# Performance work log

Measured on AMD Instinct MI355X. Metric: run time of the kernel, lower is better.

Reference implementation:

```python
import jax, jax.numpy as jnp
import numpy as np

D = 1024
H = 16
DK = D // H
MLP = 4096
EPS = 1e-5


def layernorm(x, w, b):
    mu = jnp.mean(x, axis=-1, keepdims=True)
    var = jnp.mean(jnp.square(x - mu), axis=-1, keepdims=True)
    return (x - mu) * jax.lax.rsqrt(var + EPS) * w + b


def setup_inputs() -> dict:
    key = jax.random.key(0)
    ks = jax.random.split(key, 12)
    s = 0.02
    return {
        "x": jax.random.normal(ks[0], (8, 1024, D), dtype=jnp.float32),
        "ln1_w": jnp.ones((D,), jnp.float32),
        "ln1_b": jnp.zeros((D,), jnp.float32),
        "wq": jax.random.normal(ks[1], (D, D), jnp.float32) * s,
        "bq": jnp.zeros((D,), jnp.float32),
        "wk": jax.random.normal(ks[2], (D, D), jnp.float32) * s,
        "bk": jnp.zeros((D,), jnp.float32),
        "wv": jax.random.normal(ks[3], (D, D), jnp.float32) * s,
        "bv": jnp.zeros((D,), jnp.float32),
        "wo": jax.random.normal(ks[4], (D, D), jnp.float32) * s,
        "bo": jnp.zeros((D,), jnp.float32),
        "ln2_w": jnp.ones((D,), jnp.float32),
        "ln2_b": jnp.zeros((D,), jnp.float32),
        "w1": jax.random.normal(ks[5], (D, MLP), jnp.float32) * s,
        "b1": jnp.zeros((MLP,), jnp.float32),
        "w2": jax.random.normal(ks[6], (MLP, D), jnp.float32) * s,
        "b2": jnp.zeros((D,), jnp.float32),
    }


def reference(x, ln1_w, ln1_b, wq, bq, wk, bk, wv, bv, wo, bo, ln2_w, ln2_b, w1, b1, w2, b2):
    B, S, _ = x.shape
    h = layernorm(x, ln1_w, ln1_b)
    # QKV projections, split heads: [B, H, S, DK]
    q = (h @ wq + bq).reshape(B, S, H, DK).transpose(0, 2, 1, 3)
    k = (h @ wk + bk).reshape(B, S, H, DK).transpose(0, 2, 1, 3)
    v = (h @ wv + bv).reshape(B, S, H, DK).transpose(0, 2, 1, 3)
    scores = jnp.einsum('bhqd,bhkd->bhqk', q, k) / np.sqrt(DK).astype(np.float32)
    attn = jax.nn.softmax(scores, axis=-1)
    ctx = jnp.einsum('bhqk,bhkd->bhqd', attn, v)
    ctx = ctx.transpose(0, 2, 1, 3).reshape(B, S, D)
    # NOTE: original MultiHeadAttention applies ReLU after the output projection
    attn_out = jax.nn.relu(ctx @ wo + bo)
    out1 = x + attn_out  # dropout is identity in eval
    h2 = layernorm(out1, ln2_w, ln2_b)
    ff = jax.nn.gelu(h2 @ w1 + b1, approximate=False) @ w2 + b2
    return out1 + ff
```

## Files before the change

kernel.cpp:

```cpp
#include <hip/hip_runtime.h>
#include <hip/hip_bf16.h>
#include <math.h>

typedef __bf16 bf16x8 __attribute__((ext_vector_type(8)));
typedef float f32x4 __attribute__((ext_vector_type(4)));

typedef __attribute__((address_space(3))) unsigned int lds_u32_t;
typedef __attribute__((address_space(1))) const unsigned int glb_u32_t;

static __device__ __forceinline__ f32x4 mfma16(bf16x8 a, bf16x8 b, f32x4 c) {
  return __builtin_amdgcn_mfma_f32_16x16x32_bf16(a, b, c, 0, 0, 0);
}

static __device__ __forceinline__ void load_lds16(const __bf16* g, __bf16* l) {
  __builtin_amdgcn_global_load_lds((glb_u32_t*)g, (lds_u32_t*)l, 16, 0, 0);
}

__global__ __launch_bounds__(256) void transpose_w(const float* __restrict__ src,
                                                   __bf16* __restrict__ dst,
                                                   int R, int C) {
  __shared__ float tile[32][33];
  int tx = threadIdx.x, ty = threadIdx.y;
  int c0 = blockIdx.x * 32, r0 = blockIdx.y * 32;
#pragma unroll
  for (int i = 0; i < 4; i++)
    tile[ty + 8 * i][tx] = src[(size_t)(r0 + ty + 8 * i) * C + c0 + tx];
  __syncthreads();
#pragma unroll
  for (int i = 0; i < 4; i++)
    dst[(size_t)(c0 + ty + 8 * i) * R + r0 + tx] = (__bf16)tile[tx][ty + 8 * i];
}

__global__ __launch_bounds__(256) void ln_kernel(const float* __restrict__ x,
                                                 const float* __restrict__ w,
                                                 const float* __restrict__ b,
                                                 __bf16* __restrict__ out) {
  int row = blockIdx.x, tid = threadIdx.x;
  const float* xr = x + (size_t)row * 1024;
  float v[4];
  float s = 0.f, sq = 0.f;
#pragma unroll
  for (int i = 0; i < 4; i++) {
    v[i] = xr[tid + 256 * i];
    s += v[i];
    sq += v[i] * v[i];
  }
#pragma unroll
  for (int off = 1; off < 64; off <<= 1) {
    s += __shfl_xor(s, off, 64);
    sq += __shfl_xor(sq, off, 64);
  }
  __shared__ float red[8];
  int wave = tid >> 6, lane = tid & 63;
  if (lane == 0) { red[wave] = s; red[4 + wave] = sq; }
  __syncthreads();
  if (tid == 0) {
    float S = red[0] + red[1] + red[2] + red[3];
    float SQ = red[4] + red[5] + red[6] + red[7];
    float mu = S * (1.f / 1024.f);
    float var = SQ * (1.f / 1024.f) - mu * mu;
    red[0] = mu;
    red[1] = rsqrtf(var + 1e-5f);
  }
  __syncthreads();
  float mu = red[0], rstd = red[1];
  __bf16* orow = out + (size_t)row * 1024;
#pragma unroll
  for (int i = 0; i < 4; i++) {
    int c = tid + 256 * i;
    orow[c] = (__bf16)((v[i] - mu) * rstd * w[c] + b[c]);
  }
}

enum { MODE_QKV = 0, MODE_WO = 3, MODE_F1 = 4, MODE_F2 = 5 };

template <int MODE>
__global__ __launch_bounds__(256, 2) void gemm_bt(const __bf16* __restrict__ A,
                                                  const __bf16* __restrict__ Bt,
                                                  const float* __restrict__ b0,
                                                  const float* __restrict__ b1,
                                                  const float* __restrict__ b2,
                                                  const float* __restrict__ aux,
                                                  void* __restrict__ o0,
                                                  void* __restrict__ o1,
                                                  void* __restrict__ o2,
                                                  int N, int K) {
  __shared__ __align__(16) __bf16 As[128 * 64];
  __shared__ __align__(16) __bf16 Bs[128 * 64];
  const int tid = threadIdx.x;
  const int m0 = blockIdx.y * 128, n0 = blockIdx.x * 128;
  const int wave = tid >> 6, lane = tid & 63, quad = lane >> 4, l16 = lane & 15;
  const int wm = (wave >> 1) * 64, wn = (wave & 1) * 64;

  int srow[4], sgran[4];
#pragma unroll
  for (int i = 0; i < 4; i++) {
    int inst = wave * 4 + i;
    srow[i] = inst * 8 + (lane >> 3);
    sgran[i] = (lane & 7) ^ (srow[i] & 7);
  }

  const f32x4 zero4 = {0.f, 0.f, 0.f, 0.f};
  f32x4 acc[4][4];
#pragma unroll
  for (int i = 0; i < 4; i++)
#pragma unroll
    for (int j = 0; j < 4; j++) acc[i][j] = zero4;

  for (int kt = 0; kt < K; kt += 64) {
#pragma unroll
    for (int i = 0; i < 4; i++) {
      int inst = wave * 4 + i;
      load_lds16(&A[(size_t)(m0 + srow[i]) * K + kt + sgran[i] * 8], &As[inst * 512]);
      load_lds16(&Bt[(size_t)(n0 + srow[i]) * K + kt + sgran[i] * 8], &Bs[inst * 512]);
    }
    __syncthreads();
#pragma unroll
    for (int ks = 0; ks < 64; ks += 32) {
      bf16x8 af[4], bfv[4];
#pragma unroll
      for (int mi = 0; mi < 4; mi++) {
        int row = wm + 16 * mi + l16;
        int pg = ((ks >> 3) + quad) ^ (row & 7);
        af[mi] = *(const bf16x8*)&As[row * 64 + pg * 8];
      }
#pragma unroll
      for (int ni = 0; ni < 4; ni++) {
        int row = wn + 16 * ni + l16;
        int pg = ((ks >> 3) + quad) ^ (row & 7);
        bfv[ni] = *(const bf16x8*)&Bs[row * 64 + pg * 8];
      }
#pragma unroll
      for (int mi = 0; mi < 4; mi++)
#pragma unroll
        for (int ni = 0; ni < 4; ni++)
          acc[mi][ni] = mfma16(af[mi], bfv[ni], acc[mi][ni]);
    }
    __syncthreads();
  }

  int seg = (n0 >> 10);
  const float* bsel = (MODE == MODE_QKV) ? (seg == 0 ? b0 : seg == 1 ? b1 : b2) : b0;

#pragma unroll
  for (int mi = 0; mi < 4; mi++) {
#pragma unroll
    for (int ni = 0; ni < 4; ni++) {
      int ncol = n0 + wn + 16 * ni + l16;
      int cc = ncol & 1023;
      float bval = bsel[(MODE == MODE_QKV) ? cc : ncol];
#pragma unroll
      for (int r = 0; r < 4; r++) {
        int m = m0 + wm + 16 * mi + quad * 4 + r;
        float val = acc[mi][ni][r] + bval;
        if constexpr (MODE == MODE_QKV) {
          int bb = m >> 10, s = m & 1023, h = cc >> 6, dk = cc & 63;
          if (seg == 0)
            ((__bf16*)o0)[(((size_t)(bb * 16 + h)) * 1024 + s) * 64 + dk] =
                (__bf16)(val * 0.125f);
          else if (seg == 1)
            ((__bf16*)o1)[(((size_t)(bb * 16 + h)) * 1024 + s) * 64 + dk] = (__bf16)val;
          else
            ((__bf16*)o2)[(((size_t)(bb * 16 + h)) * 64 + dk) * 1024 + s] = (__bf16)val;
        } else if constexpr (MODE == MODE_WO) {
          val = fmaxf(val, 0.f);
          size_t idx = (size_t)m * 1024 + ncol;
          ((float*)o0)[idx] = aux[idx] + val;
        } else if constexpr (MODE == MODE_F1) {
          float g = 0.5f * val * (1.f + erff(val * 0.70710678118654752f));
          ((__bf16*)o0)[(size_t)m * 4096 + ncol] = (__bf16)g;
        } else {
          size_t idx = (size_t)m * 1024 + ncol;
          ((float*)o0)[idx] = aux[idx] + val;
        }
      }
    }
  }
}

__global__ __launch_bounds__(256) void attn_kernel(const __bf16* __restrict__ Q,
                                                   const __bf16* __restrict__ Kp,
                                                   const __bf16* __restrict__ Vt,
                                                   __bf16* __restrict__ ctx) {
  __shared__ __align__(16) __bf16 Ps[128][72];
  const int tid = threadIdx.x;
  const int bh = blockIdx.x, qb = blockIdx.y;
  const int wave = tid >> 6, lane = tid & 63, quad = lane >> 4, l16 = lane & 15;
  const int qrow0 = qb * 128 + wave * 32;

  bf16x8 aq[2][2];
#pragma unroll
  for (int mi = 0; mi < 2; mi++) {
    const __bf16* qrow = Q + ((size_t)bh * 1024 + qrow0 + mi * 16 + l16) * 64;
    aq[mi][0] = *(const bf16x8*)&qrow[8 * quad];
    aq[mi][1] = *(const bf16x8*)&qrow[32 + 8 * quad];
  }

  const f32x4 zero4 = {0.f, 0.f, 0.f, 0.f};
  f32x4 o[2][4];
  float lp[2][4];
#pragma unroll
  for (int mi = 0; mi < 2; mi++)
#pragma unroll
    for (int i = 0; i < 4; i++) { o[mi][i] = zero4; lp[mi][i] = 0.f; }

  const __bf16* kb0 = Kp + (size_t)bh * 65536;
  const __bf16* vb0 = Vt + (size_t)bh * 65536;

  bf16x8 kfA[4][2], kfB[4][2];
#pragma unroll
  for (int ni = 0; ni < 4; ni++) {
    const __bf16* krow = kb0 + (16 * ni + l16) * 64;
    kfA[ni][0] = *(const bf16x8*)&krow[8 * quad];
    kfA[ni][1] = *(const bf16x8*)&krow[32 + 8 * quad];
  }

  auto body = [&](int kbk, bf16x8 (&kcur)[4][2], bf16x8 (&knxt)[4][2]) {
    bf16x8 vf[4][2];
#pragma unroll
    for (int ni = 0; ni < 4; ni++) {
      const __bf16* vrow = vb0 + (size_t)(16 * ni + l16) * 1024 + kbk * 64;
      vf[ni][0] = *(const bf16x8*)&vrow[8 * quad];
      vf[ni][1] = *(const bf16x8*)&vrow[32 + 8 * quad];
    }
    if (kbk < 15) {
      const __bf16* kbase = kb0 + (kbk + 1) * 4096;
#pragma unroll
      for (int ni = 0; ni < 4; ni++) {
        const __bf16* krow = kbase + (16 * ni + l16) * 64;
        knxt[ni][0] = *(const bf16x8*)&krow[8 * quad];
        knxt[ni][1] = *(const bf16x8*)&krow[32 + 8 * quad];
      }
    }
    f32x4 s[2][4];
#pragma unroll
    for (int mi = 0; mi < 2; mi++)
#pragma unroll
      for (int ni = 0; ni < 4; ni++) {
        s[mi][ni] = mfma16(aq[mi][0], kcur[ni][0], zero4);
        s[mi][ni] = mfma16(aq[mi][1], kcur[ni][1], s[mi][ni]);
      }
#pragma unroll
    for (int mi = 0; mi < 2; mi++)
#pragma unroll
      for (int ni = 0; ni < 4; ni++)
#pragma unroll
        for (int r = 0; r < 4; r++) {
          float p = __expf(s[mi][ni][r]);
          lp[mi][r] += p;
          Ps[wave * 32 + mi * 16 + quad * 4 + r][16 * ni + l16] = (__bf16)p;
        }
    bf16x8 pa[2][2];
#pragma unroll
    for (int mi = 0; mi < 2; mi++) {
      pa[mi][0] = *(const bf16x8*)&Ps[wave * 32 + mi * 16 + l16][8 * quad];
      pa[mi][1] = *(const bf16x8*)&Ps[wave * 32 + mi * 16 + l16][32 + 8 * quad];
    }
#pragma unroll
    for (int mi = 0; mi < 2; mi++)
#pragma unroll
      for (int ni = 0; ni < 4; ni++) {
        o[mi][ni] = mfma16(pa[mi][0], vf[ni][0], o[mi][ni]);
        o[mi][ni] = mfma16(pa[mi][1], vf[ni][1], o[mi][ni]);
      }
  };

  for (int kbk2 = 0; kbk2 < 16; kbk2 += 2) {
    body(kbk2, kfA, kfB);
    body(kbk2 + 1, kfB, kfA);
  }

#pragma unroll
  for (int mi = 0; mi < 2; mi++)
#pragma unroll
    for (int r = 0; r < 4; r++)
#pragma unroll
      for (int off = 1; off < 16; off <<= 1)
        lp[mi][r] += __shfl_xor(lp[mi][r], off, 64);

  int bb = bh >> 4, h = bh & 15;
#pragma unroll
  for (int mi = 0; mi < 2; mi++)
#pragma unroll
    for (int r = 0; r < 4; r++) {
      float inv = 1.f / lp[mi][r];
      int s = qrow0 + mi * 16 + quad * 4 + r;
#pragma unroll
      for (int ni = 0; ni < 4; ni++) {
        ctx[((size_t)(bb * 1024 + s)) * 1024 + h * 64 + 16 * ni + l16] =
            (__bf16)(o[mi][ni][r] * inv);
      }
    }
}

extern "C" void kernel_launch(void* const* d_in, const int* in_sizes, int n_in,
                              void* d_out, int out_size, void* d_ws, size_t ws_size,
                              hipStream_t stream) {
  const float* x = (const float*)d_in[0];
  const float* ln1w = (const float*)d_in[1];
  const float* ln1b = (const float*)d_in[2];
  const float* wq = (const float*)d_in[3];
  const float* bq = (const float*)d_in[4];
  const float* wk = (const float*)d_in[5];
  const float* bk = (const float*)d_in[6];
  const float* wv = (const float*)d_in[7];
  const float* bv = (const float*)d_in[8];
  const float* wo = (const float*)d_in[9];
  const float* bo = (const float*)d_in[10];
  const float* ln2w = (const float*)d_in[11];
  const float* ln2b = (const float*)d_in[12];
  const float* w1 = (const float*)d_in[13];
  const float* b1 = (const float*)d_in[14];
  const float* w2 = (const float*)d_in[15];
  const float* b2 = (const float*)d_in[16];
  float* out = (float*)d_out;

  char* ws = (char*)d_ws;
  const size_t MB = 1024 * 1024;
  __bf16* wqkv_t = (__bf16*)(ws + 0 * MB);
  __bf16* wq_t = (__bf16*)(ws + 0 * MB);
  __bf16* wk_t = (__bf16*)(ws + 2 * MB);
  __bf16* wv_t = (__bf16*)(ws + 4 * MB);
  __bf16* wo_t = (__bf16*)(ws + 6 * MB);
  __bf16* w1_t = (__bf16*)(ws + 8 * MB);
  __bf16* w2_t = (__bf16*)(ws + 16 * MB);
  __bf16* hbuf = (__bf16*)(ws + 24 * MB);
  __bf16* qbuf = (__bf16*)(ws + 40 * MB);
  __bf16* kbuf = (__bf16*)(ws + 56 * MB);
  __bf16* vtbuf = (__bf16*)(ws + 72 * MB);
  __bf16* ctxbuf = (__bf16*)(ws + 88 * MB);
  __bf16* ff1 = (__bf16*)(ws + 40 * MB);

  dim3 tb(32, 8);
  transpose_w<<<dim3(32, 32), tb, 0, stream>>>(wq, wq_t, 1024, 1024);
  transpose_w<<<dim3(32, 32), tb, 0, stream>>>(wk, wk_t, 1024, 1024);
  transpose_w<<<dim3(32, 32), tb, 0, stream>>>(wv, wv_t, 1024, 1024);
  transpose_w<<<dim3(32, 32), tb, 0, stream>>>(wo, wo_t, 1024, 1024);
  transpose_w<<<dim3(128, 32), tb, 0, stream>>>(w1, w1_t, 1024, 4096);
  transpose_w<<<dim3(32, 128), tb, 0, stream>>>(w2, w2_t, 4096, 1024);

  ln_kernel<<<8192, 256, 0, stream>>>(x, ln1w, ln1b, hbuf);

  gemm_bt<MODE_QKV><<<dim3(24, 64), 256, 0, stream>>>(
      hbuf, wqkv_t, bq, bk, bv, nullptr, qbuf, kbuf, vtbuf, 3072, 1024);

  attn_kernel<<<dim3(128, 8), 256, 0, stream>>>(qbuf, kbuf, vtbuf, ctxbuf);

  gemm_bt<MODE_WO><<<dim3(8, 64), 256, 0, stream>>>(
      ctxbuf, wo_t, bo, nullptr, nullptr, x, out, nullptr, nullptr, 1024, 1024);

  ln_kernel<<<8192, 256, 0, stream>>>(out, ln2w, ln2b, hbuf);

  gemm_bt<MODE_F1><<<dim3(32, 64), 256, 0, stream>>>(
      hbuf, w1_t, b1, nullptr, nullptr, nullptr, ff1, nullptr, nullptr, 4096, 1024);
  gemm_bt<MODE_F2><<<dim3(8, 64), 256, 0, stream>>>(
      ff1, w2_t, b2, nullptr, nullptr, out, out, nullptr, nullptr, 1024, 4096);
}
```

Baseline: 580.4 us.

## Keep attention probabilities in registers via transposed S and 16x16x16 PV MFMA

The attention kernel now computes S transposed (K as the A operand, Q as B), so each lane's accumulator already matches the A-operand layout the PV MFMA needs. That removes the LDS round-trip for P and the shared array entirely. The PV product uses the older 16x16x16 bf16 MFMA on 4-element fragments, which takes twice as many MFMA issues as before. The V loads become narrower 8-byte loads, and the row-sum reduction now needs a cross-quad shuffle plus a broadcast shuffle in the epilogue.

```diff
diff --git a/kernel.cpp b/kernel.cpp
--- a/kernel.cpp
+++ b/kernel.cpp
@@ -4,12 +4,26 @@
 
 typedef __bf16 bf16x8 __attribute__((ext_vector_type(8)));
 typedef float f32x4 __attribute__((ext_vector_type(4)));
+typedef short short4v __attribute__((ext_vector_type(4)));
 
 typedef __attribute__((address_space(3))) unsigned int lds_u32_t;
 typedef __attribute__((address_space(1))) const unsigned int glb_u32_t;
 
 static __device__ __forceinline__ f32x4 mfma16(bf16x8 a, bf16x8 b, f32x4 c) {
   return __builtin_amdgcn_mfma_f32_16x16x32_bf16(a, b, c, 0, 0, 0);
+}
+
+static __device__ __forceinline__ f32x4 pv_mfma(short4v p, short4v v, f32x4 c) {
+#if __has_builtin(__builtin_amdgcn_mfma_f32_16x16x16bf16_1k)
+  return __builtin_amdgcn_mfma_f32_16x16x16bf16_1k(p, v, c, 0, 0, 0);
+#else
+  union { short s[8]; bf16x8 v8; } a, b;
+  a.s[0] = p.x; a.s[1] = p.y; a.s[2] = p.z; a.s[3] = p.w;
+  a.s[4] = a.s[5] = a.s[6] = a.s[7] = 0;
+  b.s[0] = v.x; b.s[1] = v.y; b.s[2] = v.z; b.s[3] = v.w;
+  b.s[4] = b.s[5] = b.s[6] = b.s[7] = 0;
+  return __builtin_amdgcn_mfma_f32_16x16x32_bf16(a.v8, b.v8, c, 0, 0, 0);
+#endif
 }
 
 static __device__ __forceinline__ void load_lds16(const __bf16* g, __bf16* l) {
@@ -182,7 +196,6 @@
                                                    const __bf16* __restrict__ Kp,
                                                    const __bf16* __restrict__ Vt,
                                                    __bf16* __restrict__ ctx) {
-  __shared__ __align__(16) __bf16 Ps[128][72];
   const int tid = threadIdx.x;
   const int bh = blockIdx.x, qb = blockIdx.y;
   const int wave = tid >> 6, lane = tid & 63, quad = lane >> 4, l16 = lane & 15;
@@ -198,11 +211,11 @@
 
   const f32x4 zero4 = {0.f, 0.f, 0.f, 0.f};
   f32x4 o[2][4];
-  float lp[2][4];
+  float lp[2] = {0.f, 0.f};
 #pragma unroll
   for (int mi = 0; mi < 2; mi++)
 #pragma unroll
-    for (int i = 0; i < 4; i++) { o[mi][i] = zero4; lp[mi][i] = 0.f; }
+    for (int nj = 0; nj < 4; nj++) o[mi][nj] = zero4;
 
   const __bf16* kb0 = Kp + (size_t)bh * 65536;
   const __bf16* vb0 = Vt + (size_t)bh * 65536;
@@ -216,13 +229,13 @@
   }
 
   auto body = [&](int kbk, bf16x8 (&kcur)[4][2], bf16x8 (&knxt)[4][2]) {
-    bf16x8 vf[4][2];
-#pragma unroll
-    for (int ni = 0; ni < 4; ni++) {
-      const __bf16* vrow = vb0 + (size_t)(16 * ni + l16) * 1024 + kbk * 64;
-      vf[ni][0] = *(const bf16x8*)&vrow[8 * quad];
-      vf[ni][1] = *(const bf16x8*)&vrow[32 + 8 * quad];
-    }
+    short4v vf[4][4];
+#pragma unroll
+    for (int ni = 0; ni < 4; ni++)
+#pragma unroll
+      for (int nj = 0; nj < 4; nj++)
+        vf[ni][nj] = *(const short4v*)(vb0 + (size_t)(nj * 16 + l16) * 1024 +
+                                       kbk * 64 + ni * 16 + 4 * quad);
     if (kbk < 15) {
       const __bf16* kbase = kb0 + (kbk + 1) * 4096;
 #pragma unroll
@@ -232,37 +245,32 @@
         knxt[ni][1] = *(const bf16x8*)&krow[32 + 8 * quad];
       }
     }
-    f32x4 s[2][4];
+    f32x4 st[2][4];
 #pragma unroll
     for (int mi = 0; mi < 2; mi++)
 #pragma unroll
       for (int ni = 0; ni < 4; ni++) {
-        s[mi][ni] = mfma16(aq[mi][0], kcur[ni][0], zero4);
-        s[mi][ni] = mfma16(aq[mi][1], kcur[ni][1], s[mi][ni]);
-      }
+        st[mi][ni] = mfma16(kcur[ni][0], aq[mi][0], zero4);
+        st[mi][ni] = mfma16(kcur[ni][1], aq[mi][1], st[mi][ni]);
+      }
+    union { short4v s4; __bf16 b[4]; } pf[2][4];
 #pragma unroll
     for (int mi = 0; mi < 2; mi++)
 #pragma unroll
       for (int ni = 0; ni < 4; ni++)
 #pragma unroll
         for (int r = 0; r < 4; r++) {
-          float p = __expf(s[mi][ni][r]);
-          lp[mi][r] += p;
-          Ps[wave * 32 + mi * 16 + quad * 4 + r][16 * ni + l16] = (__bf16)p;
+          float p = __expf(st[mi][ni][r]);
+          lp[mi] += p;
+          pf[mi][ni].b[r] = (__bf16)p;
         }
-    bf16x8 pa[2][2];
-#pragma unroll
-    for (int mi = 0; mi < 2; mi++) {
-      pa[mi][0] = *(const bf16x8*)&Ps[wave * 32 + mi * 16 + l16][8 * quad];
-      pa[mi][1] = *(const bf16x8*)&Ps[wave * 32 + mi * 16 + l16][32 + 8 * quad];
-    }
-#pragma unroll
-    for (int mi = 0; mi < 2; mi++)
-#pragma unroll
-      for (int ni = 0; ni < 4; ni++) {
-        o[mi][ni] = mfma16(pa[mi][0], vf[ni][0], o[mi][ni]);
-        o[mi][ni] = mfma16(pa[mi][1], vf[ni][1], o[mi][ni]);
-      }
+#pragma unroll
+    for (int ni = 0; ni < 4; ni++)
+#pragma unroll
+      for (int mi = 0; mi < 2; mi++)
+#pragma unroll
+        for (int nj = 0; nj < 4; nj++)
+          o[mi][nj] = pv_mfma(pf[mi][ni].s4, vf[ni][nj], o[mi][nj]);
   };
 
   for (int kbk2 = 0; kbk2 < 16; kbk2 += 2) {
@@ -271,25 +279,22 @@
   }
 
 #pragma unroll
+  for (int mi = 0; mi < 2; mi++) {
+    lp[mi] += __shfl_xor(lp[mi], 16, 64);
+    lp[mi] += __shfl_xor(lp[mi], 32, 64);
+  }
+
+  int bb = bh >> 4, h = bh & 15;
+#pragma unroll
   for (int mi = 0; mi < 2; mi++)
 #pragma unroll
-    for (int r = 0; r < 4; r++)
-#pragma unroll
-      for (int off = 1; off < 16; off <<= 1)
-        lp[mi][r] += __shfl_xor(lp[mi][r], off, 64);
-
-  int bb = bh >> 4, h = bh & 15;
-#pragma unroll
-  for (int mi = 0; mi < 2; mi++)
-#pragma unroll
     for (int r = 0; r < 4; r++) {
-      float inv = 1.f / lp[mi][r];
-      int s = qrow0 + mi * 16 + quad * 4 + r;
-#pragma unroll
-      for (int ni = 0; ni < 4; ni++) {
-        ctx[((size_t)(bb * 1024 + s)) * 1024 + h * 64 + 16 * ni + l16] =
-            (__bf16)(o[mi][ni][r] * inv);
-      }
+      float inv = 1.f / __shfl(lp[mi], 4 * quad + r, 64);
+      int s = qrow0 + mi * 16 + 4 * quad + r;
+#pragma unroll
+      for (int nj = 0; nj < 4; nj++)
+        ctx[((size_t)(bb * 1024 + s)) * 1024 + h * 64 + nj * 16 + l16] =
+            (__bf16)(o[mi][nj][r] * inv);
     }
 }
 
```

Result: slower. 632.7 us (+9.0%).
